# Kernel optimization log

Hardware: AMD Instinct MI355X
Metric: run time of the kernel (lower is better)

The kernel has to match this reference:

```python
import jax, jax.numpy as jnp
import numpy as np

B, N, C, D, UP, KNN, MULT, PH = 4, 2048, 256, 64, 4, 20, 4, 64
EPS = 1e-5


def conv1d(x, w, b):
    # x: (B, Cin, N), w: (Cout, Cin)
    return jnp.einsum('oc,bcn->bon', w, x) + b[None, :, None]


def conv2d(x, w, b):
    # x: (B, Cin, N, K), 1x1 conv
    return jnp.einsum('oc,bcnk->bonk', w, x) + b[None, :, None, None]


def bn2d(x, g, bt, rm, rv):
    # eval-mode BatchNorm2d with running stats
    inv = jax.lax.rsqrt(rv + EPS)
    return g[None, :, None, None] * (x - rm[None, :, None, None]) * inv[None, :, None, None] + bt[None, :, None, None]


def group(f, idx):
    # f: (B, C, N), idx: (B, N, K) -> (B, C, N, K)
    return jax.vmap(lambda fb, ib: fb[:, ib])(f, idx)


def setup_inputs() -> dict:
    k0 = jax.random.key(0)
    ks = iter(jax.random.split(k0, 48))
    nx = lambda: next(ks)
    rn = lambda shape, s=0.05: jax.random.normal(nx(), shape, dtype=jnp.float32) * s
    z = lambda n: jnp.zeros((n,), jnp.float32)
    o = lambda n: jnp.ones((n,), jnp.float32)
    inp = {
        'pos': jax.random.normal(nx(), (B, 3, N), dtype=jnp.float32),
        'key': jax.random.normal(nx(), (B, C, N), dtype=jnp.float32),
        'query': jax.random.normal(nx(), (B, C, N), dtype=jnp.float32),
        # MLP_Res (mlp_v): in_dim=2C, hidden=C, out=C
        'wv1': rn((C, 2 * C)), 'bv1': z(C),
        'wv2': rn((C, C)), 'bv2': z(C),
        'wvs': rn((C, 2 * C)), 'bvs': z(C),
        # key/query/value projections to dim D
        'wk': rn((D, C)), 'bk': z(D),
        'wq': rn((D, C)), 'bq': z(D),
        'wval': rn((D, C)), 'bval': z(D),
        # pos_mlp: Conv2d(3,PH) -> BN -> ReLU -> Conv2d(PH,D)
        'pw1': rn((PH, 3)), 'pb1': z(PH), 'pg': o(PH), 'pbt': z(PH), 'prm': z(PH), 'prv': o(PH),
        'pw2': rn((D, PH)), 'pb2': z(D),
        # attn_mlp: Conv2d(D, D*MULT) -> BN -> ReLU -> ConvTranspose2d(D*MULT, D, (UP,1), (UP,1))
        'aw1': rn((D * MULT, D)), 'ab1': z(D * MULT), 'ag': o(D * MULT), 'abt': z(D * MULT), 'arm': z(D * MULT), 'arv': o(D * MULT),
        'ctw': rn((D * MULT, D, UP)), 'ctb': z(D),
        # conv_end: Conv1d(D, C)
        'we': rn((C, D)), 'be': z(C),
    }
    return inp


def reference(pos, key, query, wv1, bv1, wv2, bv2, wvs, bvs, wk, bk, wq, bq, wval, bval,
              pw1, pb1, pg, pbt, prm, prv, pw2, pb2,
              aw1, ab1, ag, abt, arm, arv, ctw, ctb, we, be):
    # mlp_v (MLP_Res) on concat([key, query])
    x = jnp.concatenate([key, query], axis=1)  # (B, 2C, N)
    value = conv1d(jax.nn.relu(conv1d(x, wv1, bv1)), wv2, bv2) + conv1d(x, wvs, bvs)  # (B, C, N)
    identity = value

    k_f = conv1d(key, wk, bk)      # (B, D, N)
    q_f = conv1d(query, wq, bq)    # (B, D, N)
    v_f = conv1d(value, wval, bval)

    # KNN (include_self=True): smallest-KNN indices of pairwise sq distance
    p = jnp.transpose(pos, (0, 2, 1))  # (B, N, 3)
    sq = jnp.sum(p * p, axis=-1)
    dist = sq[:, :, None] + sq[:, None, :] - 2.0 * jnp.einsum('bnc,bmc->bnm', p, p)
    idx = jax.lax.top_k(-dist, KNN)[1]  # (B, N, KNN)

    k_g = group(k_f, idx)                              # (B, D, N, KNN)
    qk_rel = q_f[:, :, :, None] - k_g
    pos_rel = pos[:, :, :, None] - group(pos, idx)     # (B, 3, N, KNN)

    h = jax.nn.relu(bn2d(conv2d(pos_rel, pw1, pb1), pg, pbt, prm, prv))
    pos_emb = conv2d(h, pw2, pb2)                      # (B, D, N, KNN)

    a = jax.nn.relu(bn2d(conv2d(qk_rel + pos_emb, aw1, ab1), ag, abt, arm, arv))  # (B, D*MULT, N, KNN)
    # ConvTranspose2d with kernel=(UP,1), stride=(UP,1): non-overlapping, out[b,o,n*UP+r,k]
    ct = jnp.einsum('bcnk,cor->bornk', a, ctw)         # (B, D, UP, N, KNN)
    Bv = a.shape[0]
    ct = jnp.transpose(ct, (0, 1, 3, 2, 4)).reshape(Bv, D, N * UP, KNN) + ctb[None, :, None, None]
    attn = jax.nn.softmax(ct, axis=-1)                 # softmax over neighbors

    v_g = group(v_f, idx) + pos_emb                    # (B, D, N, KNN)
    v_up = jnp.repeat(v_g, UP, axis=2)                 # nearest Upsample (UP,1)
    agg = jnp.sum(attn * v_up, axis=-1)                # (B, D, N*UP)
    y = conv1d(agg, we, be)                            # (B, C, N*UP)
    return y + jnp.repeat(identity, UP, axis=2)
```

## Files before the change

### kernel.cpp

```cpp
#include <hip/hip_runtime.h>
#include <hip/hip_bf16.h>

#define Bq 4
#define Nq 2048
#define Cq 256
#define Dq 64
#define UPq 4
#define KNNq 20
#define PHq 64
#define DMq 256
#define PTS 16

typedef __attribute__((ext_vector_type(8))) short short8;
typedef __attribute__((ext_vector_type(4))) short short4v;
typedef __attribute__((ext_vector_type(4))) float f32x4;
typedef __hip_bfloat16 bf16;

__device__ __forceinline__ unsigned short f2b(float x){
  bf16 h = __float2bfloat16(x);
  return *reinterpret_cast<unsigned short*>(&h);
}
__device__ __forceinline__ float b2f(short s){
  return __bfloat162float(*reinterpret_cast<bf16*>(&s));
}

__device__ __forceinline__ void swz(const float* __restrict__ src,
                                    short* __restrict__ dst,
                                    int M, int K, int g, bool transp)
{
  int j = g & 7, lane = (g >> 3) & 63, rest = g >> 9;
  int KS = K >> 5;
  int ks = rest % KS, mt = rest / KS;
  int m = mt*16 + (lane & 15);
  int k = ks*32 + ((lane >> 4) << 3) + j;
  float v = transp ? src[k*M + m] : src[m*K + k];
  dst[g] = (short)f2b(v);
}

__device__ __forceinline__ void swz_s(const float* __restrict__ src,
                                      short* __restrict__ dst,
                                      int M, int K, int g,
                                      const float* __restrict__ gam,
                                      const float* __restrict__ var)
{
  int j = g & 7, lane = (g >> 3) & 63, rest = g >> 9;
  int KS = K >> 5;
  int ks = rest % KS, mt = rest / KS;
  int m = mt*16 + (lane & 15);
  int k = ks*32 + ((lane >> 4) << 3) + j;
  float sc = gam[m] * rsqrtf(var[m] + 1e-5f);
  dst[g] = (short)f2b(src[m*K + k] * sc);
}

__global__ __launch_bounds__(256) void k_prep(
    const float* __restrict__ aw1, const float* __restrict__ ctw,
    const float* __restrict__ wv1, const float* __restrict__ wvs,
    const float* __restrict__ wv2, const float* __restrict__ wk,
    const float* __restrict__ wq,  const float* __restrict__ wval,
    const float* __restrict__ pw2, const float* __restrict__ we,
    short* __restrict__ aw1b, short* __restrict__ ctwT,
    short* __restrict__ wv1b, short* __restrict__ wvsb,
    short* __restrict__ wv2b, short* __restrict__ wkb,
    short* __restrict__ wqb,  short* __restrict__ wvalb,
    short* __restrict__ pw2b, short* __restrict__ web,
    const float* __restrict__ ag, const float* __restrict__ arv)
{
  const int t = threadIdx.x, bidx = blockIdx.x;
  if (bidx < 512){
    swz(wv1, wv1b, 256, 512, bidx*256 + t, false);
  } else if (bidx < 1024){
    swz(wvs, wvsb, 256, 512, (bidx-512)*256 + t, false);
  } else if (bidx < 1280){
    swz(wv2, wv2b, 256, 256, (bidx-1024)*256 + t, false);
  } else if (bidx < 1344){
    swz(wk, wkb, 64, 256, (bidx-1280)*256 + t, false);
  } else if (bidx < 1408){
    swz(wq, wqb, 64, 256, (bidx-1344)*256 + t, false);
  } else if (bidx < 1472){
    swz(wval, wvalb, 64, 256, (bidx-1408)*256 + t, false);
  } else if (bidx < 1488){
    swz(pw2, pw2b, 64, 64, (bidx-1472)*256 + t, false);
  } else if (bidx < 1552){
    swz_s(aw1, aw1b, 256, 64, (bidx-1488)*256 + t, ag, arv);
  } else if (bidx < 1616){
    swz(we, web, 256, 64, (bidx-1552)*256 + t, false);
  } else {
    swz(ctw, ctwT, 256, 256, (bidx-1616)*256 + t, true);
  }
}

__global__ __launch_bounds__(256) void k_value(
    const float* __restrict__ key, const float* __restrict__ query,
    const short* __restrict__ wv1b, const short* __restrict__ wvsb,
    const short* __restrict__ wv2b, const short* __restrict__ wkb,
    const short* __restrict__ wqb,  const short* __restrict__ wvalb,
    const float* __restrict__ bv1, const float* __restrict__ bv2,
    const float* __restrict__ bvs, const float* __restrict__ bk,
    const float* __restrict__ bq,  const float* __restrict__ bval,
    float* __restrict__ valueT, short* __restrict__ kfT,
    short* __restrict__ qfT,    short* __restrict__ vfT)
{
  __shared__ __align__(16) short Xb[16*520];
  __shared__ __align__(16) short hidB[16*264];
  __shared__ __align__(16) short valB[16*264];
  __shared__ __align__(16) float valF[16*264];
  const int t = threadIdx.x;
  const int b = blockIdx.x >> 7;
  const int n0 = (blockIdx.x & 127) * PTS;
  const int lane = t & 63, quad = lane >> 4, l15 = lane & 15, w = t >> 6;

  {
    const int c4 = t >> 2, pq = t & 3;
    #pragma unroll
    for (int pass=0; pass<4; pass++){
      int c = pass*64 + c4;
      float4 kv = *reinterpret_cast<const float4*>(key   + ((size_t)(b*Cq+c))*Nq + n0 + pq*4);
      float4 qv = *reinterpret_cast<const float4*>(query + ((size_t)(b*Cq+c))*Nq + n0 + pq*4);
      const float* kf_ = (const float*)&kv;
      const float* qf_ = (const float*)&qv;
      #pragma unroll
      for (int i=0;i<4;i++){
        Xb[(pq*4+i)*520 + c]       = (short)f2b(kf_[i]);
        Xb[(pq*4+i)*520 + 256 + c] = (short)f2b(qf_[i]);
      }
    }
  }
  __syncthreads();

  f32x4 acc1[4], accS[4];
  #pragma unroll
  for (int jm=0;jm<4;jm++){ acc1[jm]=(f32x4)0.f; accS[jm]=(f32x4)0.f; }

  #pragma unroll
  for (int ks=0;ks<16;ks++){
    const int kcol = ks*32 + quad*8;
    short8 xb = *reinterpret_cast<const short8*>(&Xb[l15*520 + kcol]);
    #pragma unroll
    for (int jm=0;jm<4;jm++){
      int mt = w*4 + jm;
      short8 a1 = *reinterpret_cast<const short8*>(wv1b + ((mt*16+ks)*64 + lane)*8);
      short8 as = *reinterpret_cast<const short8*>(wvsb + ((mt*16+ks)*64 + lane)*8);
      acc1[jm] = __builtin_amdgcn_mfma_f32_16x16x32_bf16(a1, xb, acc1[jm], 0,0,0);
      accS[jm] = __builtin_amdgcn_mfma_f32_16x16x32_bf16(as, xb, accS[jm], 0,0,0);
    }
  }
  #pragma unroll
  for (int jm=0;jm<4;jm++){
    #pragma unroll
    for (int r=0;r<4;r++){
      int h = (w*4+jm)*16 + quad*4 + r;
      hidB[l15*264 + h] = (short)f2b(fmaxf(acc1[jm][r] + bv1[h], 0.f));
    }
  }
  __syncthreads();

  #pragma unroll
  for (int ks=0;ks<8;ks++){
    const int kcol = ks*32 + quad*8;
    short8 hb = *reinterpret_cast<const short8*>(&hidB[l15*264 + kcol]);
    #pragma unroll
    for (int jm=0;jm<4;jm++){
      int mt = w*4 + jm;
      short8 a = *reinterpret_cast<const short8*>(wv2b + ((mt*8+ks)*64 + lane)*8);
      accS[jm] = __builtin_amdgcn_mfma_f32_16x16x32_bf16(a, hb, accS[jm], 0,0,0);
    }
  }
  #pragma unroll
  for (int jm=0;jm<4;jm++){
    #pragma unroll
    for (int r=0;r<4;r++){
      int c = (w*4+jm)*16 + quad*4 + r;
      float v = accS[jm][r] + bv2[c] + bvs[c];
      valF[l15*264 + c] = v;
      valB[l15*264 + c] = (short)f2b(v);
    }
  }
  __syncthreads();

  #pragma unroll
  for (int p=0;p<PTS;p++)
    valueT[((size_t)(b*Nq + n0 + p))*Cq + t] = valF[p*264 + t];

  {
    f32x4 pk4=(f32x4)0.f, pq4=(f32x4)0.f, pv4=(f32x4)0.f;
    #pragma unroll
    for (int ks=0;ks<8;ks++){
      const int kcol = ks*32 + quad*8;
      short8 xk = *reinterpret_cast<const short8*>(&Xb[l15*520 + kcol]);
      short8 xq = *reinterpret_cast<const short8*>(&Xb[l15*520 + 256 + kcol]);
      short8 xv = *reinterpret_cast<const short8*>(&valB[l15*264 + kcol]);
      short8 ak = *reinterpret_cast<const short8*>(wkb  + ((w*8+ks)*64 + lane)*8);
      short8 aq = *reinterpret_cast<const short8*>(wqb  + ((w*8+ks)*64 + lane)*8);
      short8 av = *reinterpret_cast<const short8*>(wvalb+ ((w*8+ks)*64 + lane)*8);
      pk4 = __builtin_amdgcn_mfma_f32_16x16x32_bf16(ak, xk, pk4, 0,0,0);
      pq4 = __builtin_amdgcn_mfma_f32_16x16x32_bf16(aq, xq, pq4, 0,0,0);
      pv4 = __builtin_amdgcn_mfma_f32_16x16x32_bf16(av, xv, pv4, 0,0,0);
    }
    short4v ok, oq, ov;
    #pragma unroll
    for (int r=0;r<4;r++){
      int o = w*16 + quad*4 + r;
      ok[r] = (short)f2b(pk4[r] + bk[o]);
      oq[r] = (short)f2b(pq4[r] + bq[o]);
      ov[r] = (short)f2b(pv4[r] + bval[o]);
    }
    int n = n0 + l15;
    size_t base = ((size_t)(b*Nq+n))*Dq + w*16 + quad*4;
    *reinterpret_cast<short4v*>(kfT + base) = ok;
    *reinterpret_cast<short4v*>(qfT + base) = oq;
    *reinterpret_cast<short4v*>(vfT + base) = ov;
  }
}

__global__ __launch_bounds__(256) void k_knn(const float* __restrict__ pos,
                                             int* __restrict__ idxT)
{
  const int t = threadIdx.x;
  const int lane = t & 63;
  const int w = t >> 6;
  const int pid = blockIdx.x*4 + w;
  const int b = pid >> 11;
  const int n = pid & (Nq-1);
  const float* px = pos + (size_t)(b*3+0)*Nq;
  const float* py = pos + (size_t)(b*3+1)*Nq;
  const float* pz = pos + (size_t)(b*3+2)*Nq;
  const float xn=px[n], yn=py[n], zn=pz[n];
  const float sqn = __fadd_rn(__fadd_rn(__fmul_rn(xn,xn),__fmul_rn(yn,yn)),__fmul_rn(zn,zn));

  double kd[32];
  #pragma unroll
  for (int i=0;i<32;i++){
    int j = i*64 + lane;
    float x=px[j], y=py[j], z=pz[j];
    float sqj = __fadd_rn(__fadd_rn(__fmul_rn(x,x),__fmul_rn(y,y)),__fmul_rn(z,z));
    float dot = __fadd_rn(__fadd_rn(__fmul_rn(xn,x),__fmul_rn(yn,y)),__fmul_rn(zn,z));
    float d   = __fsub_rn(__fadd_rn(sqn,sqj), __fmul_rn(2.0f,dot));
    unsigned u = __float_as_uint(d);
    u ^= ((unsigned)((int)u >> 31)) | 0x80000000u;
    kd[i] = (double)u * 2048.0 + (double)j;
  }

  const double BIG = 9.0e15;
  double last = -1.0;
  for (int s=0;s<KNNq;s++){
    double c[16];
    #pragma unroll
    for (int i=0;i<16;i++){
      double a0 = (kd[i]    > last) ? kd[i]    : BIG;
      double a1 = (kd[i+16] > last) ? kd[i+16] : BIG;
      c[i] = fmin(a0, a1);
    }
    #pragma unroll
    for (int off=8; off>0; off>>=1){
      #pragma unroll
      for (int i=0;i<off;i++) c[i] = fmin(c[i], c[i+off]);
    }
    double m = c[0];
    #pragma unroll
    for (int off=1; off<64; off<<=1)
      m = fmin(m, __shfl_xor(m, off));
    if (lane == 0){
      unsigned long long kk = (unsigned long long)m;
      idxT[(size_t)pid*KNNq + s] = (int)(kk & 2047ull);
    }
    last = m;
  }
}

#define UADDR(row, colb) ((((row)*128 + (colb)) ^ (((row)&7)<<4)))
#define SADDR(row, colb) ((((row)*256 + (colb)) ^ (((row)&7)<<4)))

__global__ __launch_bounds__(256, 4) void k_attn(
  const float* __restrict__ pos,
  const float* __restrict__ valueT, const short* __restrict__ kfT,
  const short* __restrict__ qfT,    const short* __restrict__ vfT,
  const int* __restrict__ idxT,
  const float* __restrict__ pw1, const float* __restrict__ pb1,
  const float* __restrict__ pg,  const float* __restrict__ pbt,
  const float* __restrict__ prm, const float* __restrict__ prv,
  const short* __restrict__ pw2b, const float* __restrict__ pb2,
  const short* __restrict__ aw1b, const float* __restrict__ ab1,
  const float* __restrict__ ag,  const float* __restrict__ abt,
  const float* __restrict__ arm, const float* __restrict__ arv,
  const short* __restrict__ ctwT,
  const short* __restrict__ web,  const float* __restrict__ be,
  float* __restrict__ out)
{
  __shared__ __align__(16) char unionA[22528];
  __shared__ __align__(16) char unionB[6144];
  __shared__ __align__(16) char unionC[6144];
  __shared__ __align__(16) short vgB[64*42];

  float* sh2S = (float*)(unionA + 12288);
  float* prl  = (float*)unionC;
  int*   nb   = (int*)(unionC + 576);

  const int t = threadIdx.x;
  const int b  = blockIdx.x >> 10;
  const int n0 = (blockIdx.x & 1023) * 2;
  const int lane = t & 63, quad = lane >> 4, l15 = lane & 15, w = t >> 6;
  const size_t bN = (size_t)b * Nq;
  const int obase = w*16 + quad*4;

  if (t < 48){
    int p = (t >= 24);
    int k = t - p*24;
    int nn = n0 + p;
    int j = (k < KNNq) ? idxT[(bN + nn)*KNNq + k] : nn;
    nb[t] = j;
    #pragma unroll
    for (int d=0; d<3; d++){
      prl[d*48+t] = pos[((size_t)(b*3+d))*Nq + nn] - pos[((size_t)(b*3+d))*Nq + j];
    }
  }
  {
    float sc = ag[t] * rsqrtf(arv[t] + 1e-5f);
    sh2S[t]  = ab1[t]*sc + (abt[t] - arm[t]*sc);
  }
  __syncthreads();

  short4v pq4[3], pk4[3], pv4[3];
  #pragma unroll
  for (int nt=0; nt<3; nt++){
    int pk = nt*16 + l15;
    int p  = (pk >= 24);
    int j  = nb[pk];
    pq4[nt] = *reinterpret_cast<const short4v*>(qfT + (bN + n0 + p)*Dq + obase);
    pk4[nt] = *reinterpret_cast<const short4v*>(kfT + (bN + j)*Dq + obase);
    pv4[nt] = *reinterpret_cast<const short4v*>(vfT + (bN + j)*Dq + obase);
  }

  {
    const int ph = t & 63;
    float sc = pg[ph] * rsqrtf(prv[ph] + 1e-5f);
    float w0 = pw1[ph*3+0]*sc, w1 = pw1[ph*3+1]*sc, w2 = pw1[ph*3+2]*sc;
    float bb = pb1[ph]*sc + (pbt[ph] - prm[ph]*sc);
    #pragma unroll
    for (int m=0;m<12;m++){
      int pk = w + m*4;
      float h = fmaf(w0, prl[pk], fmaf(w1, prl[48+pk], fmaf(w2, prl[96+pk], bb)));
      *(short*)(unionB + UADDR(pk, ph*2)) = (short)f2b(fmaxf(h, 0.f));
    }
  }
  __syncthreads();

  {
    f32x4 accP[3];
    #pragma unroll
    for (int nt=0;nt<3;nt++) accP[nt]=(f32x4)0.f;
    #pragma unroll
    for (int ks=0;ks<2;ks++){
      const int kcolb = (ks*32 + quad*8)*2;
      short8 a = *reinterpret_cast<const short8*>(pw2b + ((w*2+ks)*64 + lane)*8);
      #pragma unroll
      for (int nt=0;nt<3;nt++){
        short8 bb = *reinterpret_cast<const short8*>(unionB + UADDR(nt*16+l15, kcolb));
        accP[nt] = __builtin_amdgcn_mfma_f32_16x16x32_bf16(a, bb, accP[nt], 0,0,0);
      }
    }
    #pragma unroll
    for (int nt=0;nt<3;nt++){
      int pk = nt*16 + l15;
      bool vld = (pk < 20) || (pk >= 24 && pk < 44);
      int col  = pk - (pk >= 24 ? 4 : 0);
      short4v ut4;
      #pragma unroll
      for (int r=0;r<4;r++){
        int o = obase + r;
        float pe = accP[nt][r] + pb2[o];
        ut4[r] = (short)f2b((b2f(pq4[nt][r]) - b2f(pk4[nt][r])) + pe);
        if (vld) vgB[o*42 + col] = (short)f2b(b2f(pv4[nt][r]) + pe);
      }
      *(short4v*)(unionC + UADDR(pk, obase*2)) = ut4;
    }
  }
  __syncthreads();

  f32x4 accT[4][3];
  #pragma unroll
  for (int jm=0;jm<4;jm++)
    #pragma unroll
    for (int nt=0;nt<3;nt++) accT[jm][nt]=(f32x4)0.f;

  #pragma unroll
  for (int ch=0; ch<2; ch++){
    f32x4 accC[2][3];
    #pragma unroll
    for (int jm=0;jm<2;jm++)
      #pragma unroll
      for (int nt=0;nt<3;nt++) accC[jm][nt]=(f32x4)0.f;
    __builtin_amdgcn_s_setprio(1);
    #pragma unroll
    for (int ks=0;ks<2;ks++){
      const int kcolb = (ks*32 + quad*8)*2;
      short8 bb[3];
      #pragma unroll
      for (int nt=0;nt<3;nt++)
        bb[nt] = *reinterpret_cast<const short8*>(unionC + UADDR(nt*16+l15, kcolb));
      #pragma unroll
      for (int jm=0;jm<2;jm++){
        int mt = ch*8 + w*2 + jm;
        short8 a = *reinterpret_cast<const short8*>(aw1b + ((mt*2+ks)*64 + lane)*8);
        #pragma unroll
        for (int nt=0;nt<3;nt++)
          accC[jm][nt] = __builtin_amdgcn_mfma_f32_16x16x32_bf16(a, bb[nt], accC[jm][nt], 0,0,0);
      }
    }
    __builtin_amdgcn_s_setprio(0);

    short8 actw0[4];
    #pragma unroll
    for (int jm=0;jm<4;jm++)
      actw0[jm] = *reinterpret_cast<const short8*>(ctwT + (((w*4+jm)*8 + ch*4)*64 + lane)*8);

    if (ch == 1) __syncthreads();
    #pragma unroll
    for (int jm=0;jm<2;jm++){
      const int colb = ((w*2+jm)*16 + quad*4)*2;
      #pragma unroll
      for (int nt=0;nt<3;nt++){
        int pk = nt*16 + l15;
        short4v pkv;
        #pragma unroll
        for (int r=0;r<4;r++){
          int c = ch*128 + (w*2+jm)*16 + quad*4 + r;
          pkv[r] = (short)f2b(fmaxf(accC[jm][nt][r] + sh2S[c], 0.f));
        }
        *(short4v*)(unionA + SADDR(pk, colb)) = pkv;
      }
    }
    __syncthreads();
    __builtin_amdgcn_s_setprio(1);
    #pragma unroll
    for (int ksl=0; ksl<4; ksl++){
      const int kcolb = (ksl*32 + quad*8)*2;
      short8 bb[3];
      #pragma unroll
      for (int nt=0;nt<3;nt++)
        bb[nt] = *reinterpret_cast<const short8*>(unionA + SADDR(nt*16+l15, kcolb));
      #pragma unroll
      for (int jm=0;jm<4;jm++){
        int mt = w*4 + jm;
        short8 a = (ksl == 0) ? actw0[jm]
                 : *reinterpret_cast<const short8*>(ctwT + ((mt*8 + ch*4 + ksl)*64 + lane)*8);
        #pragma unroll
        for (int nt=0;nt<3;nt++)
          accT[jm][nt] = __builtin_amdgcn_mfma_f32_16x16x32_bf16(a, bb[nt], accT[jm][nt], 0,0,0);
      }
    }
    __builtin_amdgcn_s_setprio(0);
  }
  __syncthreads();

  #pragma unroll
  for (int nt=0;nt<3;nt++){
    int pk = nt*16 + l15;
    bool vld = (pk < 20) || (pk >= 24 && pk < 44);
    int col  = pk - (pk >= 24 ? 4 : 0);
    if (vld){
      #pragma unroll
      for (int jm=0;jm<4;jm++){
        #pragma unroll
        for (int r=0;r<4;r++){
          int row = (w*4+jm)*16 + quad*4 + r;
          *(short*)(unionA + row*88 + col*2) = (short)f2b(accT[jm][nt][r]);
        }
      }
    }
  }
  __syncthreads();

  float4 idv[4];
  if (l15 < 8){
    int p = l15 >> 2;
    #pragma unroll
    for (int jm=0;jm<4;jm++)
      idv[jm] = *reinterpret_cast<const float4*>(valueT + (bN + n0 + p)*Cq + (w*4+jm)*16 + quad*4);
  }
  short8 aweb[2][4];
  #pragma unroll
  for (int ks=0;ks<2;ks++)
    #pragma unroll
    for (int jm=0;jm<4;jm++)
      aweb[ks][jm] = *reinterpret_cast<const short8*>(web + (((w*4+jm)*2+ks)*64 + lane)*8);
  {
    const int o = t >> 2, rr = t & 3;
    #pragma unroll
    for (int p=0;p<2;p++){
      float ct[20];
      #pragma unroll
      for (int q=0;q<5;q++){
        short4v cv = *reinterpret_cast<const short4v*>(unionA + t*88 + p*40 + q*8);
        #pragma unroll
        for (int i=0;i<4;i++) ct[q*4+i] = b2f(cv[i]);
      }
      float m = ct[0];
      #pragma unroll
      for (int k=1;k<20;k++) m = fmaxf(m, ct[k]);
      float s = 0.f, a = 0.f;
      #pragma unroll
      for (int q=0;q<5;q++){
        short4v vv = *reinterpret_cast<const short4v*>((const char*)vgB + o*84 + p*40 + q*8);
        #pragma unroll
        for (int i=0;i<4;i++){
          float e = __expf(ct[q*4+i] - m);
          s += e;
          a = fmaf(e, b2f(vv[i]), a);
        }
      }
      *(short*)(unionB + UADDR(p*4+rr, o*2)) = (short)f2b(__fdividef(a, s));
    }
  }
  __syncthreads();

  {
    f32x4 accE[4];
    #pragma unroll
    for (int jm=0;jm<4;jm++) accE[jm]=(f32x4)0.f;
    __builtin_amdgcn_s_setprio(1);
    #pragma unroll
    for (int ks=0;ks<2;ks++){
      const int kcolb = (ks*32 + quad*8)*2;
      short8 bb = *reinterpret_cast<const short8*>(unionB + UADDR(l15, kcolb));
      #pragma unroll
      for (int jm=0;jm<4;jm++){
        accE[jm] = __builtin_amdgcn_mfma_f32_16x16x32_bf16(aweb[ks][jm], bb, accE[jm], 0,0,0);
      }
    }
    __builtin_amdgcn_s_setprio(0);
    if (l15 < 8){
      int p = l15 >> 2, rr = l15 & 3;
      #pragma unroll
      for (int jm=0;jm<4;jm++){
        float4 b4 = *reinterpret_cast<const float4*>(be + (w*4+jm)*16 + quad*4);
        #pragma unroll
        for (int r=0;r<4;r++){
          int c = (w*4+jm)*16 + quad*4 + r;
          float y = accE[jm][r] + ((const float*)&b4)[r] + ((const float*)&idv[jm])[r];
          out[((size_t)(b*Cq+c))*((size_t)Nq*UPq) + (size_t)(n0+p)*UPq + rr] = y;
        }
      }
    }
  }
}

extern "C" void kernel_launch(void* const* d_in, const int* in_sizes, int n_in,
                              void* d_out, int out_size, void* d_ws, size_t ws_size,
                              hipStream_t stream)
{
  const float* pos  = (const float*)d_in[0];
  const float* key  = (const float*)d_in[1];
  const float* qry  = (const float*)d_in[2];
  const float* wv1  = (const float*)d_in[3];
  const float* bv1  = (const float*)d_in[4];
  const float* wv2  = (const float*)d_in[5];
  const float* bv2  = (const float*)d_in[6];
  const float* wvs  = (const float*)d_in[7];
  const float* bvs  = (const float*)d_in[8];
  const float* wk   = (const float*)d_in[9];
  const float* bk   = (const float*)d_in[10];
  const float* wq   = (const float*)d_in[11];
  const float* bq   = (const float*)d_in[12];
  const float* wval = (const float*)d_in[13];
  const float* bval = (const float*)d_in[14];
  const float* pw1  = (const float*)d_in[15];
  const float* pb1  = (const float*)d_in[16];
  const float* pg   = (const float*)d_in[17];
  const float* pbt  = (const float*)d_in[18];
  const float* prm  = (const float*)d_in[19];
  const float* prv  = (const float*)d_in[20];
  const float* pw2  = (const float*)d_in[21];
  const float* pb2  = (const float*)d_in[22];
  const float* aw1  = (const float*)d_in[23];
  const float* ab1  = (const float*)d_in[24];
  const float* ag   = (const float*)d_in[25];
  const float* abt  = (const float*)d_in[26];
  const float* arm  = (const float*)d_in[27];
  const float* arv  = (const float*)d_in[28];
  const float* ctw  = (const float*)d_in[29];
  const float* we   = (const float*)d_in[31];
  const float* be   = (const float*)d_in[32];

  char* ws = (char*)d_ws;
  float* valueT = (float*)(ws);
  short* kfT    = (short*)(ws + 8388608);
  short* qfT    = (short*)(ws + 9437184);
  short* vfT    = (short*)(ws + 10485760);
  int*   idxT   = (int*)  (ws + 11534336);
  short* aw1b   = (short*)(ws + 12189696);
  short* ctwT   = (short*)(ws + 12222464);
  short* wv1b   = (short*)(ws + 12353536);
  short* wvsb   = (short*)(ws + 12615680);
  short* wv2b   = (short*)(ws + 12877824);
  short* wkb    = (short*)(ws + 13008896);
  short* wqb    = (short*)(ws + 13041664);
  short* wvalb  = (short*)(ws + 13074432);
  short* pw2b   = (short*)(ws + 13107200);
  short* web    = (short*)(ws + 13115392);
  float* out    = (float*)d_out;

  k_prep<<<dim3(1872), dim3(256), 0, stream>>>(
      aw1, ctw, wv1, wvs, wv2, wk, wq, wval, pw2, we,
      aw1b, ctwT, wv1b, wvsb, wv2b, wkb, wqb, wvalb, pw2b, web,
      ag, arv);
  k_value<<<dim3(Bq*Nq/PTS), dim3(256), 0, stream>>>(
      key, qry, wv1b, wvsb, wv2b, wkb, wqb, wvalb,
      bv1, bv2, bvs, bk, bq, bval,
      valueT, kfT, qfT, vfT);
  k_knn<<<dim3(Bq*Nq/4), dim3(256), 0, stream>>>(pos, idxT);
  k_attn<<<dim3(Bq*Nq/2), dim3(256), 0, stream>>>(
      pos, valueT, kfT, qfT, vfT, idxT,
      pw1, pb1, pg, pbt, prm, prv, pw2b, pb2,
      aw1b, ab1, ag, abt, arm, arv, ctwT, web, be, out);
}
```

Measured before the change: 282.2 us.

## Merge value projection and KNN kernels into one interleaved launch

Combines the k_value and k_knn kernels into a single kernel whose grid interleaves one value-projection block with four KNN blocks, so the MFMA-heavy projection work and the FP64 selection work can share the GPU at the same time. It also writes valueT straight from registers as float4 stores, which drops the fp32 staging buffer in shared memory. It adds a launch-bounds occupancy hint as well. The trade-off is that register and LDS allocation are now sized for whichever branch needs more, which can lower occupancy for the lighter branch.

```diff
diff --git a/kernel.cpp b/kernel.cpp
--- a/kernel.cpp
+++ b/kernel.cpp
@@ -89,7 +89,7 @@
   }
 }
 
-__global__ __launch_bounds__(256) void k_value(
+__global__ __launch_bounds__(256, 4) void k_vk(
     const float* __restrict__ key, const float* __restrict__ query,
     const short* __restrict__ wv1b, const short* __restrict__ wvsb,
     const short* __restrict__ wv2b, const short* __restrict__ wkb,
@@ -98,172 +98,170 @@
     const float* __restrict__ bvs, const float* __restrict__ bk,
     const float* __restrict__ bq,  const float* __restrict__ bval,
     float* __restrict__ valueT, short* __restrict__ kfT,
-    short* __restrict__ qfT,    short* __restrict__ vfT)
+    short* __restrict__ qfT,    short* __restrict__ vfT,
+    const float* __restrict__ pos, int* __restrict__ idxT)
 {
-  __shared__ __align__(16) short Xb[16*520];
-  __shared__ __align__(16) short hidB[16*264];
-  __shared__ __align__(16) short valB[16*264];
-  __shared__ __align__(16) float valF[16*264];
   const int t = threadIdx.x;
-  const int b = blockIdx.x >> 7;
-  const int n0 = (blockIdx.x & 127) * PTS;
-  const int lane = t & 63, quad = lane >> 4, l15 = lane & 15, w = t >> 6;
-
-  {
-    const int c4 = t >> 2, pq = t & 3;
-    #pragma unroll
-    for (int pass=0; pass<4; pass++){
-      int c = pass*64 + c4;
-      float4 kv = *reinterpret_cast<const float4*>(key   + ((size_t)(b*Cq+c))*Nq + n0 + pq*4);
-      float4 qv = *reinterpret_cast<const float4*>(query + ((size_t)(b*Cq+c))*Nq + n0 + pq*4);
-      const float* kf_ = (const float*)&kv;
-      const float* qf_ = (const float*)&qv;
-      #pragma unroll
-      for (int i=0;i<4;i++){
-        Xb[(pq*4+i)*520 + c]       = (short)f2b(kf_[i]);
-        Xb[(pq*4+i)*520 + 256 + c] = (short)f2b(qf_[i]);
-      }
-    }
-  }
-  __syncthreads();
-
-  f32x4 acc1[4], accS[4];
-  #pragma unroll
-  for (int jm=0;jm<4;jm++){ acc1[jm]=(f32x4)0.f; accS[jm]=(f32x4)0.f; }
-
-  #pragma unroll
-  for (int ks=0;ks<16;ks++){
-    const int kcol = ks*32 + quad*8;
-    short8 xb = *reinterpret_cast<const short8*>(&Xb[l15*520 + kcol]);
+  const int lane = t & 63, w = t >> 6;
+  const int vb = blockIdx.x / 5, rem = blockIdx.x % 5;
+
+  if (rem == 4){
+    __shared__ __align__(16) short Xb[16*520];
+    __shared__ __align__(16) short hidB[16*264];
+    __shared__ __align__(16) short valB[16*264];
+    const int b = vb >> 7;
+    const int n0 = (vb & 127) * PTS;
+    const int quad = lane >> 4, l15 = lane & 15;
+
+    {
+      const int c4 = t >> 2, pq = t & 3;
+      #pragma unroll
+      for (int pass=0; pass<4; pass++){
+        int c = pass*64 + c4;
+        float4 kv = *reinterpret_cast<const float4*>(key   + ((size_t)(b*Cq+c))*Nq + n0 + pq*4);
+        float4 qv = *reinterpret_cast<const float4*>(query + ((size_t)(b*Cq+c))*Nq + n0 + pq*4);
+        const float* kf_ = (const float*)&kv;
+        const float* qf_ = (const float*)&qv;
+        #pragma unroll
+        for (int i=0;i<4;i++){
+          Xb[(pq*4+i)*520 + c]       = (short)f2b(kf_[i]);
+          Xb[(pq*4+i)*520 + 256 + c] = (short)f2b(qf_[i]);
+        }
+      }
+    }
+    __syncthreads();
+
+    f32x4 acc1[4], accS[4];
+    #pragma unroll
+    for (int jm=0;jm<4;jm++){ acc1[jm]=(f32x4)0.f; accS[jm]=(f32x4)0.f; }
+
+    #pragma unroll
+    for (int ks=0;ks<16;ks++){
+      const int kcol = ks*32 + quad*8;
+      short8 xb = *reinterpret_cast<const short8*>(&Xb[l15*520 + kcol]);
+      #pragma unroll
+      for (int jm=0;jm<4;jm++){
+        int mt = w*4 + jm;
+        short8 a1 = *reinterpret_cast<const short8*>(wv1b + ((mt*16+ks)*64 + lane)*8);
+        short8 as = *reinterpret_cast<const short8*>(wvsb + ((mt*16+ks)*64 + lane)*8);
+        acc1[jm] = __builtin_amdgcn_mfma_f32_16x16x32_bf16(a1, xb, acc1[jm], 0,0,0);
+        accS[jm] = __builtin_amdgcn_mfma_f32_16x16x32_bf16(as, xb, accS[jm], 0,0,0);
+      }
+    }
     #pragma unroll
     for (int jm=0;jm<4;jm++){
-      int mt = w*4 + jm;
-      short8 a1 = *reinterpret_cast<const short8*>(wv1b + ((mt*16+ks)*64 + lane)*8);
-      short8 as = *reinterpret_cast<const short8*>(wvsb + ((mt*16+ks)*64 + lane)*8);
-      acc1[jm] = __builtin_amdgcn_mfma_f32_16x16x32_bf16(a1, xb, acc1[jm], 0,0,0);
-      accS[jm] = __builtin_amdgcn_mfma_f32_16x16x32_bf16(as, xb, accS[jm], 0,0,0);
-    }
-  }
-  #pragma unroll
-  for (int jm=0;jm<4;jm++){
-    #pragma unroll
-    for (int r=0;r<4;r++){
-      int h = (w*4+jm)*16 + quad*4 + r;
-      hidB[l15*264 + h] = (short)f2b(fmaxf(acc1[jm][r] + bv1[h], 0.f));
-    }
-  }
-  __syncthreads();
-
-  #pragma unroll
-  for (int ks=0;ks<8;ks++){
-    const int kcol = ks*32 + quad*8;
-    short8 hb = *reinterpret_cast<const short8*>(&hidB[l15*264 + kcol]);
-    #pragma unroll
-    for (int jm=0;jm<4;jm++){
-      int mt = w*4 + jm;
-      short8 a = *reinterpret_cast<const short8*>(wv2b + ((mt*8+ks)*64 + lane)*8);
-      accS[jm] = __builtin_amdgcn_mfma_f32_16x16x32_bf16(a, hb, accS[jm], 0,0,0);
-    }
-  }
-  #pragma unroll
-  for (int jm=0;jm<4;jm++){
-    #pragma unroll
-    for (int r=0;r<4;r++){
-      int c = (w*4+jm)*16 + quad*4 + r;
-      float v = accS[jm][r] + bv2[c] + bvs[c];
-      valF[l15*264 + c] = v;
-      valB[l15*264 + c] = (short)f2b(v);
-    }
-  }
-  __syncthreads();
-
-  #pragma unroll
-  for (int p=0;p<PTS;p++)
-    valueT[((size_t)(b*Nq + n0 + p))*Cq + t] = valF[p*264 + t];
-
-  {
-    f32x4 pk4=(f32x4)0.f, pq4=(f32x4)0.f, pv4=(f32x4)0.f;
+      #pragma unroll
+      for (int r=0;r<4;r++){
+        int h = (w*4+jm)*16 + quad*4 + r;
+        hidB[l15*264 + h] = (short)f2b(fmaxf(acc1[jm][r] + bv1[h], 0.f));
+      }
+    }
+    __syncthreads();
+
     #pragma unroll
     for (int ks=0;ks<8;ks++){
       const int kcol = ks*32 + quad*8;
-      short8 xk = *reinterpret_cast<const short8*>(&Xb[l15*520 + kcol]);
-      short8 xq = *reinterpret_cast<const short8*>(&Xb[l15*520 + 256 + kcol]);
-      short8 xv = *reinterpret_cast<const short8*>(&valB[l15*264 + kcol]);
-      short8 ak = *reinterpret_cast<const short8*>(wkb  + ((w*8+ks)*64 + lane)*8);
-      short8 aq = *reinterpret_cast<const short8*>(wqb  + ((w*8+ks)*64 + lane)*8);
-      short8 av = *reinterpret_cast<const short8*>(wvalb+ ((w*8+ks)*64 + lane)*8);
-      pk4 = __builtin_amdgcn_mfma_f32_16x16x32_bf16(ak, xk, pk4, 0,0,0);
-      pq4 = __builtin_amdgcn_mfma_f32_16x16x32_bf16(aq, xq, pq4, 0,0,0);
-      pv4 = __builtin_amdgcn_mfma_f32_16x16x32_bf16(av, xv, pv4, 0,0,0);
-    }
-    short4v ok, oq, ov;
-    #pragma unroll
-    for (int r=0;r<4;r++){
-      int o = w*16 + quad*4 + r;
-      ok[r] = (short)f2b(pk4[r] + bk[o]);
-      oq[r] = (short)f2b(pq4[r] + bq[o]);
-      ov[r] = (short)f2b(pv4[r] + bval[o]);
-    }
-    int n = n0 + l15;
-    size_t base = ((size_t)(b*Nq+n))*Dq + w*16 + quad*4;
-    *reinterpret_cast<short4v*>(kfT + base) = ok;
-    *reinterpret_cast<short4v*>(qfT + base) = oq;
-    *reinterpret_cast<short4v*>(vfT + base) = ov;
-  }
-}
-
-__global__ __launch_bounds__(256) void k_knn(const float* __restrict__ pos,
-                                             int* __restrict__ idxT)
-{
-  const int t = threadIdx.x;
-  const int lane = t & 63;
-  const int w = t >> 6;
-  const int pid = blockIdx.x*4 + w;
-  const int b = pid >> 11;
-  const int n = pid & (Nq-1);
-  const float* px = pos + (size_t)(b*3+0)*Nq;
-  const float* py = pos + (size_t)(b*3+1)*Nq;
-  const float* pz = pos + (size_t)(b*3+2)*Nq;
-  const float xn=px[n], yn=py[n], zn=pz[n];
-  const float sqn = __fadd_rn(__fadd_rn(__fmul_rn(xn,xn),__fmul_rn(yn,yn)),__fmul_rn(zn,zn));
-
-  double kd[32];
-  #pragma unroll
-  for (int i=0;i<32;i++){
-    int j = i*64 + lane;
-    float x=px[j], y=py[j], z=pz[j];
-    float sqj = __fadd_rn(__fadd_rn(__fmul_rn(x,x),__fmul_rn(y,y)),__fmul_rn(z,z));
-    float dot = __fadd_rn(__fadd_rn(__fmul_rn(xn,x),__fmul_rn(yn,y)),__fmul_rn(zn,z));
-    float d   = __fsub_rn(__fadd_rn(sqn,sqj), __fmul_rn(2.0f,dot));
-    unsigned u = __float_as_uint(d);
-    u ^= ((unsigned)((int)u >> 31)) | 0x80000000u;
-    kd[i] = (double)u * 2048.0 + (double)j;
-  }
-
-  const double BIG = 9.0e15;
-  double last = -1.0;
-  for (int s=0;s<KNNq;s++){
-    double c[16];
-    #pragma unroll
-    for (int i=0;i<16;i++){
-      double a0 = (kd[i]    > last) ? kd[i]    : BIG;
-      double a1 = (kd[i+16] > last) ? kd[i+16] : BIG;
-      c[i] = fmin(a0, a1);
-    }
-    #pragma unroll
-    for (int off=8; off>0; off>>=1){
-      #pragma unroll
-      for (int i=0;i<off;i++) c[i] = fmin(c[i], c[i+off]);
-    }
-    double m = c[0];
-    #pragma unroll
-    for (int off=1; off<64; off<<=1)
-      m = fmin(m, __shfl_xor(m, off));
-    if (lane == 0){
-      unsigned long long kk = (unsigned long long)m;
-      idxT[(size_t)pid*KNNq + s] = (int)(kk & 2047ull);
-    }
-    last = m;
+      short8 hb = *reinterpret_cast<const short8*>(&hidB[l15*264 + kcol]);
+      #pragma unroll
+      for (int jm=0;jm<4;jm++){
+        int mt = w*4 + jm;
+        short8 a = *reinterpret_cast<const short8*>(wv2b + ((mt*8+ks)*64 + lane)*8);
+        accS[jm] = __builtin_amdgcn_mfma_f32_16x16x32_bf16(a, hb, accS[jm], 0,0,0);
+      }
+    }
+    #pragma unroll
+    for (int jm=0;jm<4;jm++){
+      const int cb = (w*4+jm)*16 + quad*4;
+      float4 v4;
+      #pragma unroll
+      for (int r=0;r<4;r++){
+        int c = cb + r;
+        float v = accS[jm][r] + bv2[c] + bvs[c];
+        ((float*)&v4)[r] = v;
+        valB[l15*264 + c] = (short)f2b(v);
+      }
+      *reinterpret_cast<float4*>(valueT + ((size_t)(b*Nq + n0 + l15))*Cq + cb) = v4;
+    }
+    __syncthreads();
+
+    {
+      f32x4 pk4=(f32x4)0.f, pq4=(f32x4)0.f, pv4=(f32x4)0.f;
+      #pragma unroll
+      for (int ks=0;ks<8;ks++){
+        const int kcol = ks*32 + quad*8;
+        short8 xk = *reinterpret_cast<const short8*>(&Xb[l15*520 + kcol]);
+        short8 xq = *reinterpret_cast<const short8*>(&Xb[l15*520 + 256 + kcol]);
+        short8 xv = *reinterpret_cast<const short8*>(&valB[l15*264 + kcol]);
+        short8 ak = *reinterpret_cast<const short8*>(wkb  + ((w*8+ks)*64 + lane)*8);
+        short8 aq = *reinterpret_cast<const short8*>(wqb  + ((w*8+ks)*64 + lane)*8);
+        short8 av = *reinterpret_cast<const short8*>(wvalb+ ((w*8+ks)*64 + lane)*8);
+        pk4 = __builtin_amdgcn_mfma_f32_16x16x32_bf16(ak, xk, pk4, 0,0,0);
+        pq4 = __builtin_amdgcn_mfma_f32_16x16x32_bf16(aq, xq, pq4, 0,0,0);
+        pv4 = __builtin_amdgcn_mfma_f32_16x16x32_bf16(av, xv, pv4, 0,0,0);
+      }
+      short4v ok, oq, ov;
+      #pragma unroll
+      for (int r=0;r<4;r++){
+        int o = w*16 + quad*4 + r;
+        ok[r] = (short)f2b(pk4[r] + bk[o]);
+        oq[r] = (short)f2b(pq4[r] + bq[o]);
+        ov[r] = (short)f2b(pv4[r] + bval[o]);
+      }
+      int n = n0 + l15;
+      size_t base = ((size_t)(b*Nq+n))*Dq + w*16 + quad*4;
+      *reinterpret_cast<short4v*>(kfT + base) = ok;
+      *reinterpret_cast<short4v*>(qfT + base) = oq;
+      *reinterpret_cast<short4v*>(vfT + base) = ov;
+    }
+  } else {
+    const int kb = vb*4 + rem;
+    const int pid = kb*4 + w;
+    const int b = pid >> 11;
+    const int n = pid & (Nq-1);
+    const float* px = pos + (size_t)(b*3+0)*Nq;
+    const float* py = pos + (size_t)(b*3+1)*Nq;
+    const float* pz = pos + (size_t)(b*3+2)*Nq;
+    const float xn=px[n], yn=py[n], zn=pz[n];
+    const float sqn = __fadd_rn(__fadd_rn(__fmul_rn(xn,xn),__fmul_rn(yn,yn)),__fmul_rn(zn,zn));
+
+    double kd[32];
+    #pragma unroll
+    for (int i=0;i<32;i++){
+      int j = i*64 + lane;
+      float x=px[j], y=py[j], z=pz[j];
+      float sqj = __fadd_rn(__fadd_rn(__fmul_rn(x,x),__fmul_rn(y,y)),__fmul_rn(z,z));
+      float dot = __fadd_rn(__fadd_rn(__fmul_rn(xn,x),__fmul_rn(yn,y)),__fmul_rn(zn,z));
+      float d   = __fsub_rn(__fadd_rn(sqn,sqj), __fmul_rn(2.0f,dot));
+      unsigned u = __float_as_uint(d);
+      u ^= ((unsigned)((int)u >> 31)) | 0x80000000u;
+      kd[i] = (double)u * 2048.0 + (double)j;
+    }
+
+    const double BIG = 9.0e15;
+    double last = -1.0;
+    for (int s=0;s<KNNq;s++){
+      double c[16];
+      #pragma unroll
+      for (int i=0;i<16;i++){
+        double a0 = (kd[i]    > last) ? kd[i]    : BIG;
+        double a1 = (kd[i+16] > last) ? kd[i+16] : BIG;
+        c[i] = fmin(a0, a1);
+      }
+      #pragma unroll
+      for (int off=8; off>0; off>>=1){
+        #pragma unroll
+        for (int i=0;i<off;i++) c[i] = fmin(c[i], c[i+off]);
+      }
+      double m = c[0];
+      #pragma unroll
+      for (int off=1; off<64; off<<=1)
+        m = fmin(m, __shfl_xor(m, off));
+      if (lane == 0){
+        unsigned long long kk = (unsigned long long)m;
+        idxT[(size_t)pid*KNNq + s] = (int)(kk & 2047ull);
+      }
+      last = m;
+    }
   }
 }
 
@@ -603,11 +601,10 @@
       aw1, ctw, wv1, wvs, wv2, wk, wq, wval, pw2, we,
       aw1b, ctwT, wv1b, wvsb, wv2b, wkb, wqb, wvalb, pw2b, web,
       ag, arv);
-  k_value<<<dim3(Bq*Nq/PTS), dim3(256), 0, stream>>>(
+  k_vk<<<dim3(2560), dim3(256), 0, stream>>>(
       key, qry, wv1b, wvsb, wv2b, wkb, wqb, wvalb,
       bv1, bv2, bvs, bk, bq, bval,
-      valueT, kfT, qfT, vfT);
-  k_knn<<<dim3(Bq*Nq/4), dim3(256), 0, stream>>>(pos, idxT);
+      valueT, kfT, qfT, vfT, pos, idxT);
   k_attn<<<dim3(Bq*Nq/2), dim3(256), 0, stream>>>(
       pos, valueT, kfT, qfT, vfT, idxT,
       pw1, pb1, pg, pbt, prm, prv, pw2b, pb2,
```

Result: faster. 270.6 us (-4.1%).
